# Kernel tuning notes

Measured on AMD Instinct MI355X. Metric: run time of the kernel, lower is better.

## Reference

```python
import jax, jax.numpy as jnp
import numpy as np

DIMS = 1024; HEAD = 16; HD = DIMS // HEAD
MAX_DIST = 1024; MAX_SPAN = 1024; TEMP_SCALE = 0.01
SCALE = HD ** -0.25  # hd^-0.25 per the torch modules


def _layer_norm(x, g, b, eps=1e-5):
    m = jnp.mean(x, -1, keepdims=True)
    v = jnp.mean((x - m) ** 2, -1, keepdims=True)
    return (x - m) * jax.lax.rsqrt(v + eps) * g + b


def _forward(x, ln_a_g, ln_a_b, ln_b_g, ln_b_b, Wq, bq, Wk, Wv, bv, Wc, bc, Wp, bp, Wo, bo):
    B, S, D = x.shape
    local = _layer_norm(x, ln_a_g, ln_a_b)
    globe = _layer_norm(x, ln_b_g, ln_b_b)
    # --- global path: QueryModule/KeyModule/ValueModule + AttentionCombiner SDPA (mask=None) ---
    q = (globe @ Wq.T + bq).reshape(B, S, HEAD, HD).transpose(0, 2, 1, 3) * SCALE
    k = (globe @ Wk.T).reshape(B, S, HEAD, HD).transpose(0, 2, 1, 3) * SCALE
    v = (globe @ Wv.T + bv).reshape(B, S, HEAD, HD).transpose(0, 2, 1, 3)
    # SDPA applies its own 1/sqrt(hd) on top of the modules' hd^-0.25 scalings (faithful to torch)
    scores = jnp.einsum('bhqd,bhkd->bhqk', q, k) / jnp.sqrt(jnp.asarray(HD, x.dtype))
    w = jax.nn.softmax(scores, -1)
    g_out = jnp.einsum('bhqk,bhkd->bhqd', w, v).transpose(0, 2, 1, 3).reshape(B, S, D)
    g_out = g_out @ Wc.T + bc
    # --- span predictor; torch uses span_scale.mean().item() which detaches -> stop_gradient ---
    span_scale = jax.nn.sigmoid(jnp.mean(g_out, 1) @ Wp.T + bp)  # [B,1]
    span_mean = jax.lax.stop_gradient(jnp.mean(span_scale))
    span_len = jnp.minimum(jnp.floor(MAX_SPAN * span_mean).astype(jnp.int32), S)
    eff = jnp.maximum(jnp.minimum(span_len, MAX_DIST), 1)  # eff_span (>=1 to keep softmax finite)
    temp = 1.0 + TEMP_SCALE * (1.0 - span_mean)  # sharpen=True branch
    # --- local AdaptiveSpan path: q[:, :eff], k[:, :eff], v[:, :eff] expressed as masking
    #     so shapes stay static under jit; rows >= eff are the zero-padding of the span output.
    lh = local.reshape(B, S, HEAD, HD).transpose(0, 2, 1, 3)  # [B,H,S,hd]
    ls = jnp.einsum('bhqd,bhkd->bhqk', lh, lh) / temp * SCALE
    valid = jnp.arange(S) < eff
    ls = jnp.where(valid[None, None, None, :], ls, jnp.asarray(-1e30, x.dtype))
    lw = jax.nn.softmax(ls, -1)
    l_out = jnp.einsum('bhqk,bhkd->bhqd', lw, lh).transpose(0, 2, 1, 3).reshape(B, S, D)
    l_out = jnp.where(valid[None, :, None], l_out, jnp.asarray(0.0, x.dtype))
    combined = jnp.concatenate([l_out, g_out], -1)  # [B,S,2D]
    return combined @ Wo.T + bo


def setup_inputs() -> dict:
    key = jax.random.key(0)
    ks = jax.random.split(key, 8)
    B, S = 2, 1024
    nrm = lambda k, sh, std=0.02: jax.random.normal(k, sh, jnp.float32) * std
    return {
        'x': jax.random.normal(ks[0], (B, S, DIMS), jnp.float32),
        'ln_a_g': jnp.ones(DIMS, jnp.float32), 'ln_a_b': jnp.zeros(DIMS, jnp.float32),
        'ln_b_g': jnp.ones(DIMS, jnp.float32), 'ln_b_b': jnp.zeros(DIMS, jnp.float32),
        'Wq': nrm(ks[1], (DIMS, DIMS)), 'bq': jnp.zeros(DIMS, jnp.float32),
        'Wk': nrm(ks[2], (DIMS, DIMS)),
        'Wv': nrm(ks[3], (DIMS, DIMS)), 'bv': jnp.zeros(DIMS, jnp.float32),
        'Wc': nrm(ks[4], (DIMS, DIMS)), 'bc': jnp.zeros(DIMS, jnp.float32),
        'Wp': nrm(ks[5], (1, DIMS), (2.0 / (DIMS + 1)) ** 0.5), 'bp': jnp.zeros(1, jnp.float32),
        'Wo': nrm(ks[6], (DIMS, 2 * DIMS)), 'bo': jnp.zeros(DIMS, jnp.float32),
    }


def reference(x, ln_a_g, ln_a_b, ln_b_g, ln_b_b, Wq, bq, Wk, Wv, bv, Wc, bc, Wp, bp, Wo, bo):
    return _forward(x, ln_a_g, ln_a_b, ln_b_g, ln_b_b, Wq, bq, Wk, Wv, bv, Wc, bc, Wp, bp, Wo, bo)
```

## Files before the change

### kernel.cpp

```cpp
#include <hip/hip_runtime.h>
#include <math.h>

#define S_LEN 1024
#define DIMS  1024
#define NHEAD 16
#define HD    64
#define BATCH 2
#define MROWS (BATCH * S_LEN)
#define LOG2E 1.44269504088896f

typedef unsigned short us;
typedef __attribute__((ext_vector_type(8))) __bf16 bf8_t;
typedef __attribute__((ext_vector_type(8))) unsigned short us8_t;
typedef __attribute__((ext_vector_type(4))) unsigned short us4_t;
typedef __attribute__((ext_vector_type(4))) float f32x4;
typedef __attribute__((ext_vector_type(4))) unsigned int u32x4;

static __device__ inline us f2bf(float f) {
    unsigned int u = __builtin_bit_cast(unsigned int, f);
    unsigned int r = u + 0x7fffu + ((u >> 16) & 1u);
    return (us)(r >> 16);
}
static __device__ inline float bf2f(us v) {
    unsigned int u = ((unsigned int)v) << 16;
    return __builtin_bit_cast(float, u);
}
static __device__ inline unsigned int pk2bf(float lo, float hi) {
    unsigned int r;
    asm("v_cvt_pk_bf16_f32 %0, %1, %2" : "=v"(r) : "v"(lo), "v"(hi));
    return r;
}
static __device__ inline f32x4 mfma16(us8_t a, us8_t b, f32x4 c) {
    return __builtin_amdgcn_mfma_f32_16x16x32_bf16(
        __builtin_bit_cast(bf8_t, a), __builtin_bit_cast(bf8_t, b), c, 0, 0, 0);
}
static __device__ __forceinline__ void gload16(const us* g, us* l) {
    __builtin_amdgcn_global_load_lds(
        (__attribute__((address_space(1))) void*)(g),
        (__attribute__((address_space(3))) void*)(l), 16, 0, 0);
}

__global__ __launch_bounds__(256) void prep_kernel(
    const float* __restrict__ s0, const float* __restrict__ s1,
    const float* __restrict__ s2, const float* __restrict__ s3,
    const float* __restrict__ s4,
    us* __restrict__ d0, us* __restrict__ d1, us* __restrict__ d2,
    us* __restrict__ d3, us* __restrict__ d4,
    const float* __restrict__ x,
    const float* __restrict__ ga, const float* __restrict__ ba,
    const float* __restrict__ gb, const float* __restrict__ bb,
    us* __restrict__ outA, us* __restrict__ outB,
    unsigned int* __restrict__ ctr)
{
    int bidx = blockIdx.x;
    int t = threadIdx.x;
    if (bidx == 0 && t == 0) *ctr = 0u;
    if (bidx < 6144) {
        const float* src; us* dst; int blk;
        if (bidx < 1024)      { src = s0; dst = d0; blk = bidx; }
        else if (bidx < 2048) { src = s1; dst = d1; blk = bidx - 1024; }
        else if (bidx < 3072) { src = s2; dst = d2; blk = bidx - 2048; }
        else if (bidx < 4096) { src = s3; dst = d3; blk = bidx - 3072; }
        else                  { src = s4; dst = d4; blk = bidx - 4096; }
        size_t idx = (size_t)blk * 1024 + t * 4;
        float4 v = *(const float4*)(src + idx);
        us4_t ot;
        ot[0] = f2bf(v.x); ot[1] = f2bf(v.y); ot[2] = f2bf(v.z); ot[3] = f2bf(v.w);
        *(us4_t*)(dst + idx) = ot;
        return;
    }
    int row = bidx - 6144;
    const float* xr = x + (size_t)row * DIMS;
    float4 v = *(const float4*)(xr + t * 4);
    float sum1 = v.x + v.y + v.z + v.w;
    float sumq = v.x * v.x + v.y * v.y + v.z * v.z + v.w * v.w;
#pragma unroll
    for (int o = 32; o > 0; o >>= 1) {
        sum1 += __shfl_down(sum1, o, 64);
        sumq += __shfl_down(sumq, o, 64);
    }
    __shared__ float rs[4], rq[4];
    int wid = t >> 6, lane = t & 63;
    if (lane == 0) { rs[wid] = sum1; rq[wid] = sumq; }
    __syncthreads();
    float T1 = rs[0] + rs[1] + rs[2] + rs[3];
    float T2 = rq[0] + rq[1] + rq[2] + rq[3];
    float mean = T1 * (1.0f / DIMS);
    float var  = T2 * (1.0f / DIMS) - mean * mean;
    float inv  = 1.0f / sqrtf(var + 1e-5f);
    float4 vga = *(const float4*)(ga + t * 4);
    float4 vba = *(const float4*)(ba + t * 4);
    float4 vgb = *(const float4*)(gb + t * 4);
    float4 vbb = *(const float4*)(bb + t * 4);
    float nx = (v.x - mean) * inv, ny = (v.y - mean) * inv;
    float nz = (v.z - mean) * inv, nw = (v.w - mean) * inv;
    us4_t oa, ob;
    oa[0] = f2bf(nx * vga.x + vba.x); oa[1] = f2bf(ny * vga.y + vba.y);
    oa[2] = f2bf(nz * vga.z + vba.z); oa[3] = f2bf(nw * vga.w + vba.w);
    ob[0] = f2bf(nx * vgb.x + vbb.x); ob[1] = f2bf(ny * vgb.y + vbb.y);
    ob[2] = f2bf(nz * vgb.z + vbb.z); ob[3] = f2bf(nw * vgb.w + vbb.w);
    *(us4_t*)(outA + (size_t)row * DIMS + t * 4) = oa;
    *(us4_t*)(outB + (size_t)row * DIMS + t * 4) = ob;
}

template <int OUTBF>
static __device__ __forceinline__ void gemm128g_body(
    const us* __restrict__ A, int lda,
    const us* __restrict__ W, int ldw,
    const float* __restrict__ bias,
    void* __restrict__ Cp, int ldc, int K,
    int bm, int bn, us* As, us* Bs)
{
    int tid = threadIdx.x;
    int w = tid >> 6, l = tid & 63, l15 = l & 15, lhi = l >> 4;
    int wr = w >> 1, wc = w & 1;
    f32x4 acc[4][2];
#pragma unroll
    for (int m = 0; m < 4; ++m) { acc[m][0] = (f32x4){0,0,0,0}; acc[m][1] = (f32x4){0,0,0,0}; }
    int lr8 = l >> 3, lc = l & 7;

    int nK = K >> 6;
    {
#pragma unroll
        for (int c = 0; c < 4; ++c) {
            int R0 = c * 32 + w * 8;
            int row = R0 + lr8;
            int col8 = lc ^ (row & 7);
            gload16(A + (size_t)(bm + row) * lda + col8 * 8, As + R0 * 64);
        }
#pragma unroll
        for (int c = 0; c < 2; ++c) {
            int R0 = c * 32 + w * 8;
            int row = R0 + lr8;
            int col8 = lc ^ (row & 7);
            gload16(W + (size_t)(bn + row) * ldw + col8 * 8, Bs + R0 * 64);
        }
    }
    for (int t = 0; t < nK; ++t) {
        int cur = t & 1;
        __syncthreads();
        if (t + 1 < nK) {
            int nxt = cur ^ 1;
            int kt = (t + 1) * 64;
#pragma unroll
            for (int c = 0; c < 4; ++c) {
                int R0 = c * 32 + w * 8;
                int row = R0 + lr8;
                int col8 = lc ^ (row & 7);
                gload16(A + (size_t)(bm + row) * lda + kt + col8 * 8,
                        As + nxt * (128 * 64) + R0 * 64);
            }
#pragma unroll
            for (int c = 0; c < 2; ++c) {
                int R0 = c * 32 + w * 8;
                int row = R0 + lr8;
                int col8 = lc ^ (row & 7);
                gload16(W + (size_t)(bn + row) * ldw + kt + col8 * 8,
                        Bs + nxt * (64 * 64) + R0 * 64);
            }
        }
        const us* Ab = As + cur * (128 * 64);
        const us* Bb = Bs + cur * (64 * 64);
#pragma unroll
        for (int kk = 0; kk < 2; ++kk) {
            int xo = ((kk * 4 + lhi) ^ (l15 & 7)) * 8;
            us8_t af[4], bfr[2];
#pragma unroll
            for (int m = 0; m < 4; ++m)
                af[m] = *(const us8_t*)&Ab[(wr * 64 + m * 16 + l15) * 64 + xo];
#pragma unroll
            for (int n = 0; n < 2; ++n)
                bfr[n] = *(const us8_t*)&Bb[(wc * 32 + n * 16 + l15) * 64 + xo];
#pragma unroll
            for (int m = 0; m < 4; ++m)
#pragma unroll
                for (int n = 0; n < 2; ++n)
                    acc[m][n] = mfma16(af[m], bfr[n], acc[m][n]);
        }
    }
    float bvv[2] = {0.f, 0.f};
    if (bias) {
#pragma unroll
        for (int n = 0; n < 2; ++n)
            bvv[n] = bias[bn + wc * 32 + n * 16 + l15];
    }
#pragma unroll
    for (int m = 0; m < 4; ++m) {
#pragma unroll
        for (int n = 0; n < 2; ++n) {
            int row = bm + wr * 64 + m * 16 + lhi * 4;
            int col = bn + wc * 32 + n * 16 + l15;
            if (OUTBF) {
                us* Cb = (us*)Cp;
                unsigned int p01 = pk2bf(acc[m][n][0] + bvv[n], acc[m][n][1] + bvv[n]);
                unsigned int p23 = pk2bf(acc[m][n][2] + bvv[n], acc[m][n][3] + bvv[n]);
                Cb[(size_t)(row + 0) * ldc + col] = (us)p01;
                Cb[(size_t)(row + 1) * ldc + col] = (us)(p01 >> 16);
                Cb[(size_t)(row + 2) * ldc + col] = (us)p23;
                Cb[(size_t)(row + 3) * ldc + col] = (us)(p23 >> 16);
            } else {
                float* Cf = (float*)Cp;
#pragma unroll
                for (int r = 0; r < 4; ++r)
                    Cf[(size_t)(row + r) * ldc + col] = acc[m][n][r] + bvv[n];
            }
        }
    }
}

__global__ __launch_bounds__(256) void gemm_qkv(
    const us* __restrict__ A,
    const us* __restrict__ Wq, const us* __restrict__ Wk, const us* __restrict__ Wv,
    const float* __restrict__ bq, const float* __restrict__ bv,
    us* __restrict__ qo, us* __restrict__ ko, us* __restrict__ vo)
{
    __shared__ __align__(16) us As[2][128 * 64];
    __shared__ __align__(16) us Bs[2][64 * 64];
    int which = blockIdx.x >> 4;
    int bn = (blockIdx.x & 15) * 64, bm = blockIdx.y * 128;
    const us* W = (which == 0) ? Wq : ((which == 1) ? Wk : Wv);
    const float* bias2 = (which == 0) ? bq : ((which == 2) ? bv : nullptr);
    us* Out = (which == 0) ? qo : ((which == 1) ? ko : vo);
    gemm128g_body<1>(A, DIMS, W, DIMS, bias2, Out, DIMS, DIMS, bm, bn,
                     &As[0][0], &Bs[0][0]);
}

template <int OUTBF>
__global__ __launch_bounds__(256) void gemm64g(
    const us* __restrict__ A, int lda,
    const us* __restrict__ W, int ldw,
    const float* __restrict__ bias,
    void* __restrict__ Cp, int ldc, int K)
{
    __shared__ __align__(16) us As[2][64 * 64];
    __shared__ __align__(16) us Bs[2][64 * 64];
    int tid = threadIdx.x;
    int w = tid >> 6, l = tid & 63, l15 = l & 15, lhi = l >> 4;
    int wr = w >> 1, wc = w & 1;
    int bm = blockIdx.y * 64, bn = blockIdx.x * 64;
    f32x4 acc[2][2] = {{{0,0,0,0},{0,0,0,0}},{{0,0,0,0},{0,0,0,0}}};
    int lr8 = l >> 3, lc = l & 7;

    int nK = K >> 6;
    {
#pragma unroll
        for (int c = 0; c < 2; ++c) {
            int R0 = c * 32 + w * 8;
            int row = R0 + lr8;
            int col8 = lc ^ (row & 7);
            gload16(A + (size_t)(bm + row) * lda + col8 * 8, &As[0][R0 * 64]);
            gload16(W + (size_t)(bn + row) * ldw + col8 * 8, &Bs[0][R0 * 64]);
        }
    }
    for (int t = 0; t < nK; ++t) {
        int cur = t & 1;
        __syncthreads();
        if (t + 1 < nK) {
            int nxt = cur ^ 1;
            int kt = (t + 1) * 64;
#pragma unroll
            for (int c = 0; c < 2; ++c) {
                int R0 = c * 32 + w * 8;
                int row = R0 + lr8;
                int col8 = lc ^ (row & 7);
                gload16(A + (size_t)(bm + row) * lda + kt + col8 * 8, &As[nxt][R0 * 64]);
                gload16(W + (size_t)(bn + row) * ldw + kt + col8 * 8, &Bs[nxt][R0 * 64]);
            }
        }
#pragma unroll
        for (int kk = 0; kk < 2; ++kk) {
            int xo = ((kk * 4 + lhi) ^ (l15 & 7)) * 8;
            us8_t af[2], bfr[2];
#pragma unroll
            for (int m = 0; m < 2; ++m)
                af[m] = *(const us8_t*)&As[cur][(wr * 32 + m * 16 + l15) * 64 + xo];
#pragma unroll
            for (int n = 0; n < 2; ++n)
                bfr[n] = *(const us8_t*)&Bs[cur][(wc * 32 + n * 16 + l15) * 64 + xo];
#pragma unroll
            for (int m = 0; m < 2; ++m)
#pragma unroll
                for (int n = 0; n < 2; ++n)
                    acc[m][n] = mfma16(af[m], bfr[n], acc[m][n]);
        }
    }
    float bvv[2] = {0.f, 0.f};
    if (bias) {
#pragma unroll
        for (int n = 0; n < 2; ++n)
            bvv[n] = bias[bn + wc * 32 + n * 16 + l15];
    }
#pragma unroll
    for (int m = 0; m < 2; ++m) {
#pragma unroll
        for (int n = 0; n < 2; ++n) {
            int row = bm + wr * 32 + m * 16 + lhi * 4;
            int col = bn + wc * 32 + n * 16 + l15;
            if (OUTBF) {
                us* Cb = (us*)Cp;
                unsigned int p01 = pk2bf(acc[m][n][0] + bvv[n], acc[m][n][1] + bvv[n]);
                unsigned int p23 = pk2bf(acc[m][n][2] + bvv[n], acc[m][n][3] + bvv[n]);
                Cb[(size_t)(row + 0) * ldc + col] = (us)p01;
                Cb[(size_t)(row + 1) * ldc + col] = (us)(p01 >> 16);
                Cb[(size_t)(row + 2) * ldc + col] = (us)p23;
                Cb[(size_t)(row + 3) * ldc + col] = (us)(p23 >> 16);
            } else {
                float* Cf = (float*)Cp;
#pragma unroll
                for (int r = 0; r < 4; ++r)
                    Cf[(size_t)(row + r) * ldc + col] = acc[m][n][r] + bvv[n];
            }
        }
    }
}

template <int LOCAL>
__global__ __launch_bounds__(512) void attn_mfma(
    const us* __restrict__ Q, const us* __restrict__ K,
    const us* __restrict__ V, us* __restrict__ O, int ldo,
    const float* __restrict__ span)
{
    __shared__ __align__(16) us Ks[2][64 * 64];
    __shared__ __align__(16) us Vt[2][64 * 64];
    __shared__ __align__(16) us Ps[8][1024];

    int bid = blockIdx.x;
    int xcd = bid & 7, slot = bid >> 3;
    int p = xcd + 8 * (slot >> 4);
    int q0blk = (slot & 15) * 64;
    int h = p & 15, b = p >> 4;

    int tid = threadIdx.x;
    int w = tid >> 6, l = tid & 63;
    int l15 = l & 15, lhi = l >> 4;
    int wq = w & 3, wk = w >> 2;

    float scale; int eff;
    if (LOCAL) { scale = span[1] * LOG2E; eff = (int)span[0]; }
    else       { scale = LOG2E / 64.0f; eff = S_LEN; }
    int ntiles = LOCAL ? ((eff + 63) >> 6) : 16;
    int nIter = (ntiles + 1) >> 1;

    int qrow = q0blk + wq * 16 + l15;
    const us* qptr = Q + ((size_t)(b * S_LEN + qrow)) * DIMS + h * HD + lhi * 8;
    us8_t qf[2];
    qf[0] = *(const us8_t*)(qptr);
    qf[1] = *(const us8_t*)(qptr + 32);

    f32x4 o[4] = {{0,0,0,0},{0,0,0,0},{0,0,0,0},{0,0,0,0}};
    float m_r[4] = {-1e30f, -1e30f, -1e30f, -1e30f};
    float l_r[4] = {0.f, 0.f, 0.f, 0.f};

    int half = tid >> 8;
    int t0 = tid & 255;
    int krow = t0 >> 3, kcol8 = t0 & 7;
    int ksl = (kcol8 ^ (krow & 7)) * 8;
    int vkb = t0 & 15, vdb = t0 >> 4;
    const us* Kb = K + ((size_t)(b * S_LEN)) * DIMS + h * HD;
    const us* Vb = V + ((size_t)(b * S_LEN)) * DIMS + h * HD;

    unsigned pbase = (unsigned)(unsigned long long)&Ps[w][0];
    unsigned paddr = pbase + (unsigned)(l * 8);

    us8_t kc0, kc1;
    us4_t vr0, vr1, vr2, vr3;
    if (half < ntiles) {
        const us* kp = Kb + (size_t)(half * 64 + krow) * DIMS + kcol8 * 8;
        kc0 = *(const us8_t*)kp;
        kc1 = *(const us8_t*)(kp + (size_t)32 * DIMS);
        const us* vp = Vb + (size_t)(half * 64 + vkb * 4) * DIMS + vdb * 4;
        vr0 = *(const us4_t*)(vp);
        vr1 = *(const us4_t*)(vp + DIMS);
        vr2 = *(const us4_t*)(vp + 2 * DIMS);
        vr3 = *(const us4_t*)(vp + 3 * DIMS);
    }

    for (int i = 0; i < nIter; ++i) {
        __syncthreads();
        if (2 * i + half < ntiles) {
            *(us8_t*)&Ks[half][krow * 64 + ksl] = kc0;
            *(us8_t*)&Ks[half][(krow + 32) * 64 + ksl] = kc1;
#pragma unroll
            for (int j = 0; j < 4; ++j) {
                int d = vdb * 4 + j;
                us4_t wv;
                wv[0] = vr0[j]; wv[1] = vr1[j]; wv[2] = vr2[j]; wv[3] = vr3[j];
                int slotv = (vkb >> 1) ^ (d & 7);
                *(us4_t*)&Vt[half][d * 64 + slotv * 8 + (vkb & 1) * 4] = wv;
            }
        }
        __syncthreads();
        int nt2 = 2 * (i + 1) + half;
        if (nt2 < ntiles) {
            const us* kp = Kb + (size_t)(nt2 * 64 + krow) * DIMS + kcol8 * 8;
            kc0 = *(const us8_t*)kp;
            kc1 = *(const us8_t*)(kp + (size_t)32 * DIMS);
            const us* vp = Vb + (size_t)(nt2 * 64 + vkb * 4) * DIMS + vdb * 4;
            vr0 = *(const us4_t*)(vp);
            vr1 = *(const us4_t*)(vp + DIMS);
            vr2 = *(const us4_t*)(vp + 2 * DIMS);
            vr3 = *(const us4_t*)(vp + 3 * DIMS);
        }
        int kt = 2 * i + wk;
        if (kt < ntiles) {
            f32x4 s4[4] = {{0,0,0,0},{0,0,0,0},{0,0,0,0},{0,0,0,0}};
            __builtin_amdgcn_s_setprio(1);
#pragma unroll
            for (int kk = 0; kk < 2; ++kk) {
                int xo = ((kk * 4 + lhi) ^ (l15 & 7)) * 8;
#pragma unroll
                for (int n = 0; n < 4; ++n) {
                    us8_t bk = *(const us8_t*)&Ks[wk][(n * 16 + l15) * 64 + xo];
                    s4[n] = mfma16(qf[kk], bk, s4[n]);
                }
            }
            __builtin_amdgcn_s_setprio(0);
#pragma unroll
            for (int n = 0; n < 4; ++n) {
                s4[n] *= scale;
                if (LOCAL) {
                    int key = kt * 64 + n * 16 + l15;
                    if (key >= eff) {
                        s4[n][0] = -1e30f; s4[n][1] = -1e30f;
                        s4[n][2] = -1e30f; s4[n][3] = -1e30f;
                    }
                }
            }
            float tl[4];
#pragma unroll
            for (int r = 0; r < 4; ++r)
                tl[r] = fmaxf(fmaxf(s4[0][r], s4[1][r]), fmaxf(s4[2][r], s4[3][r]));
            int ex = (tl[0] > m_r[0] + 11.5f) | (tl[1] > m_r[1] + 11.5f) |
                     (tl[2] > m_r[2] + 11.5f) | (tl[3] > m_r[3] + 11.5f);
            if (__any(ex)) {
#pragma unroll
                for (int msk = 1; msk <= 8; msk <<= 1) {
#pragma unroll
                    for (int r = 0; r < 4; ++r)
                        tl[r] = fmaxf(tl[r], __shfl_xor(tl[r], msk, 64));
                }
                float fac[4];
#pragma unroll
                for (int r = 0; r < 4; ++r) {
                    float mn = fmaxf(m_r[r], tl[r]);
                    fac[r] = exp2f(m_r[r] - mn);
                    m_r[r] = mn;
                    l_r[r] *= fac[r];
                }
#pragma unroll
                for (int n = 0; n < 4; ++n) {
                    o[n][0] *= fac[0]; o[n][1] *= fac[1];
                    o[n][2] *= fac[2]; o[n][3] *= fac[3];
                }
            }
#pragma unroll
            for (int n = 0; n < 4; ++n) {
                float p0 = exp2f(s4[n][0] - m_r[0]);
                float p1 = exp2f(s4[n][1] - m_r[1]);
                float p2 = exp2f(s4[n][2] - m_r[2]);
                float p3 = exp2f(s4[n][3] - m_r[3]);
                l_r[0] += p0; l_r[1] += p1; l_r[2] += p2; l_r[3] += p3;
                unsigned int p01 = pk2bf(p0, p1);
                unsigned int p23 = pk2bf(p2, p3);
                int idx = (n >> 1) * 512 + ((l15 & 4) ? 256 : 0)
                        + ((n & 1) * 2 + (l15 >> 3)) * 64 + (l15 & 3) * 16 + lhi * 4;
                *(uint2*)&Ps[w][idx] = make_uint2(p01, p23);
            }
            unsigned long long ta0, ta1, ta2, ta3;
            asm volatile(
                "ds_read_b64_tr_b16 %0, %4\n\t"
                "ds_read_b64_tr_b16 %1, %4 offset:512\n\t"
                "ds_read_b64_tr_b16 %2, %4 offset:1024\n\t"
                "ds_read_b64_tr_b16 %3, %4 offset:1536\n\t"
                "s_waitcnt lgkmcnt(0)"
                : "=&v"(ta0), "=&v"(ta1), "=&v"(ta2), "=&v"(ta3)
                : "v"(paddr)
                : "memory");
            __builtin_amdgcn_sched_barrier(0);
            u32x4 w0 = {(unsigned)ta0, (unsigned)(ta0 >> 32),
                        (unsigned)ta1, (unsigned)(ta1 >> 32)};
            u32x4 w1 = {(unsigned)ta2, (unsigned)(ta2 >> 32),
                        (unsigned)ta3, (unsigned)(ta3 >> 32)};
            us8_t pa0 = __builtin_bit_cast(us8_t, w0);
            us8_t pa1 = __builtin_bit_cast(us8_t, w1);
            __builtin_amdgcn_s_setprio(1);
#pragma unroll
            for (int kk = 0; kk < 2; ++kk) {
                int xo = ((kk * 4 + lhi) ^ (l15 & 7)) * 8;
                us8_t pa = kk ? pa1 : pa0;
#pragma unroll
                for (int n = 0; n < 4; ++n) {
                    us8_t vb = *(const us8_t*)&Vt[wk][(n * 16 + l15) * 64 + xo];
                    o[n] = mfma16(pa, vb, o[n]);
                }
            }
            __builtin_amdgcn_s_setprio(0);
        }
    }

#pragma unroll
    for (int msk = 1; msk <= 8; msk <<= 1) {
#pragma unroll
        for (int r = 0; r < 4; ++r)
            l_r[r] += __shfl_xor(l_r[r], msk, 64);
    }

    __syncthreads();
    float* obuf = (float*)&Ks[0][0];
    float* mlb  = (float*)&Vt[0][0];
    if (wk == 1) {
#pragma unroll
        for (int n = 0; n < 4; ++n)
#pragma unroll
            for (int r = 0; r < 4; ++r)
                obuf[wq * 1024 + (lhi * 4 + r) * 64 + n * 16 + l15] = o[n][r];
        if (l15 == 0) {
#pragma unroll
            for (int r = 0; r < 4; ++r) {
                mlb[wq * 32 + (lhi * 4 + r) * 2 + 0] = m_r[r];
                mlb[wq * 32 + (lhi * 4 + r) * 2 + 1] = l_r[r];
            }
        }
    }
    __syncthreads();
    if (wk == 0) {
        float f0[4], f1[4], rcp[4];
#pragma unroll
        for (int r = 0; r < 4; ++r) {
            int row = lhi * 4 + r;
            float m1 = mlb[wq * 32 + row * 2 + 0];
            float l1 = mlb[wq * 32 + row * 2 + 1];
            float ms = fmaxf(m_r[r], m1);
            f0[r] = exp2f(m_r[r] - ms);
            f1[r] = exp2f(m1 - ms);
            rcp[r] = 1.0f / (l_r[r] * f0[r] + l1 * f1[r]);
        }
#pragma unroll
        for (int n = 0; n < 4; ++n) {
            float vv[4];
#pragma unroll
            for (int r = 0; r < 4; ++r) {
                int row = q0blk + wq * 16 + lhi * 4 + r;
                float val = (o[n][r] * f0[r] +
                             obuf[wq * 1024 + (lhi * 4 + r) * 64 + n * 16 + l15] * f1[r]) * rcp[r];
                if (LOCAL && row >= eff) val = 0.0f;
                vv[r] = val;
            }
            int row0 = q0blk + wq * 16 + lhi * 4;
            unsigned int p01 = pk2bf(vv[0], vv[1]);
            unsigned int p23 = pk2bf(vv[2], vv[3]);
            size_t base = ((size_t)(b * S_LEN + row0)) * ldo + h * HD + n * 16 + l15;
            O[base + 0 * ldo] = (us)p01;
            O[base + 1 * ldo] = (us)(p01 >> 16);
            O[base + 2 * ldo] = (us)p23;
            O[base + 3 * ldo] = (us)(p23 >> 16);
        }
    }
}

__global__ __launch_bounds__(256) void span_fused(
    const us* __restrict__ gout, const float* __restrict__ Wp,
    const float* __restrict__ bp,
    float* __restrict__ partials, float* __restrict__ spanbuf,
    unsigned int* __restrict__ ctr)
{
    int slice = blockIdx.x;
    int b = blockIdx.y;
    int t = threadIdx.x;
    float4 wp = *(const float4*)(Wp + t * 4);
    float acc = 0;
    int srow0 = slice * 8;
    for (int s = srow0; s < srow0 + 8; ++s) {
        us4_t g = *(const us4_t*)(gout + (size_t)(b * S_LEN + s) * 2048 + t * 4);
        acc += bf2f(g[0]) * wp.x + bf2f(g[1]) * wp.y + bf2f(g[2]) * wp.z + bf2f(g[3]) * wp.w;
    }
#pragma unroll
    for (int o = 32; o > 0; o >>= 1) acc += __shfl_down(acc, o, 64);
    __shared__ float r[4];
    int wid = t >> 6, lane = t & 63;
    if (lane == 0) r[wid] = acc;
    __syncthreads();
    if (t == 0) {
        partials[b * 128 + slice] = r[0] + r[1] + r[2] + r[3];
        __threadfence();
        unsigned int old = atomicAdd(ctr, 1u);
        if (old == 255u) {
            __threadfence();
            float l0 = 0, l1 = 0;
            for (int i = 0; i < 128; ++i) { l0 += partials[i]; l1 += partials[128 + i]; }
            l0 = l0 * (1.0f / 1024.0f) + bp[0];
            l1 = l1 * (1.0f / 1024.0f) + bp[0];
            float sg0 = 1.0f / (1.0f + expf(-l0));
            float sg1 = 1.0f / (1.0f + expf(-l1));
            float sm = 0.5f * (sg0 + sg1);
            int sl = (int)floorf(1024.0f * sm);
            int eff = sl; if (eff > 1024) eff = 1024; if (eff < 1) eff = 1;
            float temp = 1.0f + 0.01f * (1.0f - sm);
            spanbuf[0] = (float)eff;
            spanbuf[1] = 0.35355339059327378f / temp;
        }
    }
}

extern "C" void kernel_launch(void* const* d_in, const int* in_sizes, int n_in,
                              void* d_out, int out_size, void* d_ws, size_t ws_size,
                              hipStream_t stream)
{
    (void)in_sizes; (void)n_in; (void)out_size; (void)ws_size;
    const float* x   = (const float*)d_in[0];
    const float* lag = (const float*)d_in[1];
    const float* lab = (const float*)d_in[2];
    const float* lbg = (const float*)d_in[3];
    const float* lbb = (const float*)d_in[4];
    const float* Wq  = (const float*)d_in[5];
    const float* bq  = (const float*)d_in[6];
    const float* Wk  = (const float*)d_in[7];
    const float* Wv  = (const float*)d_in[8];
    const float* bv  = (const float*)d_in[9];
    const float* Wc  = (const float*)d_in[10];
    const float* bc  = (const float*)d_in[11];
    const float* Wp  = (const float*)d_in[12];
    const float* bp  = (const float*)d_in[13];
    const float* Wo  = (const float*)d_in[14];
    const float* bo  = (const float*)d_in[15];
    float* out = (float*)d_out;
    us* wsu = (us*)d_ws;

    const size_t NM = (size_t)MROWS * DIMS;
    us* lnAbf = wsu;
    us* lnBbf = wsu + NM;
    us* gattbf = lnBbf;
    us* qbf   = wsu + 2 * NM;
    us* kbf   = wsu + 3 * NM;
    us* vbf   = wsu + 4 * NM;
    us* combbf = qbf;
    us* Wqbf  = wsu + 5 * NM;
    us* Wkbf  = Wqbf + DIMS * DIMS;
    us* Wvbf  = Wkbf + DIMS * DIMS;
    us* Wcbf  = Wvbf + DIMS * DIMS;
    us* Wobf  = Wcbf + DIMS * DIMS;
    float* partials = (float*)(Wobf + 2 * DIMS * DIMS);
    float* spanbuf  = partials + 256;
    unsigned int* spanctr = (unsigned int*)(spanbuf + 8);

    prep_kernel<<<8192, 256, 0, stream>>>(Wq, Wk, Wv, Wc, Wo,
                                          Wqbf, Wkbf, Wvbf, Wcbf, Wobf,
                                          x, lag, lab, lbg, lbb, lnAbf, lnBbf,
                                          spanctr);

    gemm_qkv<<<dim3(48, MROWS / 128), 256, 0, stream>>>(
        lnBbf, Wqbf, Wkbf, Wvbf, bq, bv, qbf, kbf, vbf);

    attn_mfma<0><<<512, 512, 0, stream>>>(qbf, kbf, vbf, gattbf, DIMS, nullptr);

    gemm64g<1><<<dim3(DIMS / 64, MROWS / 64), 256, 0, stream>>>(
        gattbf, DIMS, Wcbf, DIMS, bc, combbf + 1024, 2048, DIMS);

    span_fused<<<dim3(128, BATCH), 256, 0, stream>>>(combbf + 1024, Wp, bp,
                                                     partials, spanbuf, spanctr);

    attn_mfma<1><<<512, 512, 0, stream>>>(lnAbf, lnAbf, lnAbf, combbf, 2048, spanbuf);

    gemm64g<0><<<dim3(DIMS / 64, MROWS / 64), 256, 0, stream>>>(
        combbf, 2048, Wobf, 2048, bo, out, DIMS, 2 * DIMS);
}
```

Baseline: 128.3 us.

## Fuse span reduction into Wc GEMM and overlap local attention with Wo GEMM

Folds the span predictor's Wp dot product into the epilogue of the Wc projection GEMM, which removes the separate span kernel and its reread of the global output. The Wo projection is split by K half: the global half runs as extra blocks inside the local attention launch, and the local half runs afterwards and accumulates into the output. The aim is fewer launches and better GPU occupancy by running independent work concurrently. In exchange, the new Wo GEMM is single-buffered with no prefetch, and the read-modify-write accumulate adds extra fp32 traffic.

```diff
diff --git a/kernel.cpp b/kernel.cpp
--- a/kernel.cpp
+++ b/kernel.cpp
@@ -103,12 +103,11 @@
     *(us4_t*)(outB + (size_t)row * DIMS + t * 4) = ob;
 }
 
-template <int OUTBF>
 static __device__ __forceinline__ void gemm128g_body(
     const us* __restrict__ A, int lda,
     const us* __restrict__ W, int ldw,
     const float* __restrict__ bias,
-    void* __restrict__ Cp, int ldc, int K,
+    us* __restrict__ Cp, int ldc, int K,
     int bm, int bn, us* As, us* Bs)
 {
     int tid = threadIdx.x;
@@ -118,7 +117,6 @@
 #pragma unroll
     for (int m = 0; m < 4; ++m) { acc[m][0] = (f32x4){0,0,0,0}; acc[m][1] = (f32x4){0,0,0,0}; }
     int lr8 = l >> 3, lc = l & 7;
-
     int nK = K >> 6;
     {
 #pragma unroll
@@ -190,20 +188,12 @@
         for (int n = 0; n < 2; ++n) {
             int row = bm + wr * 64 + m * 16 + lhi * 4;
             int col = bn + wc * 32 + n * 16 + l15;
-            if (OUTBF) {
-                us* Cb = (us*)Cp;
-                unsigned int p01 = pk2bf(acc[m][n][0] + bvv[n], acc[m][n][1] + bvv[n]);
-                unsigned int p23 = pk2bf(acc[m][n][2] + bvv[n], acc[m][n][3] + bvv[n]);
-                Cb[(size_t)(row + 0) * ldc + col] = (us)p01;
-                Cb[(size_t)(row + 1) * ldc + col] = (us)(p01 >> 16);
-                Cb[(size_t)(row + 2) * ldc + col] = (us)p23;
-                Cb[(size_t)(row + 3) * ldc + col] = (us)(p23 >> 16);
-            } else {
-                float* Cf = (float*)Cp;
-#pragma unroll
-                for (int r = 0; r < 4; ++r)
-                    Cf[(size_t)(row + r) * ldc + col] = acc[m][n][r] + bvv[n];
-            }
+            unsigned int p01 = pk2bf(acc[m][n][0] + bvv[n], acc[m][n][1] + bvv[n]);
+            unsigned int p23 = pk2bf(acc[m][n][2] + bvv[n], acc[m][n][3] + bvv[n]);
+            Cp[(size_t)(row + 0) * ldc + col] = (us)p01;
+            Cp[(size_t)(row + 1) * ldc + col] = (us)(p01 >> 16);
+            Cp[(size_t)(row + 2) * ldc + col] = (us)p23;
+            Cp[(size_t)(row + 3) * ldc + col] = (us)(p23 >> 16);
         }
     }
 }
@@ -221,26 +211,27 @@
     const us* W = (which == 0) ? Wq : ((which == 1) ? Wk : Wv);
     const float* bias2 = (which == 0) ? bq : ((which == 2) ? bv : nullptr);
     us* Out = (which == 0) ? qo : ((which == 1) ? ko : vo);
-    gemm128g_body<1>(A, DIMS, W, DIMS, bias2, Out, DIMS, DIMS, bm, bn,
-                     &As[0][0], &Bs[0][0]);
-}
-
-template <int OUTBF>
-__global__ __launch_bounds__(256) void gemm64g(
-    const us* __restrict__ A, int lda,
-    const us* __restrict__ W, int ldw,
-    const float* __restrict__ bias,
-    void* __restrict__ Cp, int ldc, int K)
+    gemm128g_body(A, DIMS, W, DIMS, bias2, Out, DIMS, DIMS, bm, bn,
+                  &As[0][0], &Bs[0][0]);
+}
+
+__global__ __launch_bounds__(256) void gemm_wc_span(
+    const us* __restrict__ A, const us* __restrict__ W,
+    const float* __restrict__ bias, us* __restrict__ Cp,
+    const float* __restrict__ Wp, const float* __restrict__ bp,
+    float* __restrict__ partials, float* __restrict__ spanbuf,
+    unsigned int* __restrict__ ctr)
 {
     __shared__ __align__(16) us As[2][64 * 64];
     __shared__ __align__(16) us Bs[2][64 * 64];
+    __shared__ float red[4];
+    const int lda = DIMS, ldw = DIMS, ldc = 2048, K = DIMS;
     int tid = threadIdx.x;
     int w = tid >> 6, l = tid & 63, l15 = l & 15, lhi = l >> 4;
     int wr = w >> 1, wc = w & 1;
     int bm = blockIdx.y * 64, bn = blockIdx.x * 64;
     f32x4 acc[2][2] = {{{0,0,0,0},{0,0,0,0}},{{0,0,0,0},{0,0,0,0}}};
     int lr8 = l >> 3, lc = l & 7;
-
     int nK = K >> 6;
     {
 #pragma unroll
@@ -284,47 +275,71 @@
                     acc[m][n] = mfma16(af[m], bfr[n], acc[m][n]);
         }
     }
-    float bvv[2] = {0.f, 0.f};
-    if (bias) {
-#pragma unroll
-        for (int n = 0; n < 2; ++n)
-            bvv[n] = bias[bn + wc * 32 + n * 16 + l15];
-    }
+    float bvv[2], wpv[2];
+#pragma unroll
+    for (int n = 0; n < 2; ++n) {
+        int col = bn + wc * 32 + n * 16 + l15;
+        bvv[n] = bias[col];
+        wpv[n] = Wp[col];
+    }
+    float spart = 0.f;
 #pragma unroll
     for (int m = 0; m < 2; ++m) {
 #pragma unroll
         for (int n = 0; n < 2; ++n) {
             int row = bm + wr * 32 + m * 16 + lhi * 4;
             int col = bn + wc * 32 + n * 16 + l15;
-            if (OUTBF) {
-                us* Cb = (us*)Cp;
-                unsigned int p01 = pk2bf(acc[m][n][0] + bvv[n], acc[m][n][1] + bvv[n]);
-                unsigned int p23 = pk2bf(acc[m][n][2] + bvv[n], acc[m][n][3] + bvv[n]);
-                Cb[(size_t)(row + 0) * ldc + col] = (us)p01;
-                Cb[(size_t)(row + 1) * ldc + col] = (us)(p01 >> 16);
-                Cb[(size_t)(row + 2) * ldc + col] = (us)p23;
-                Cb[(size_t)(row + 3) * ldc + col] = (us)(p23 >> 16);
-            } else {
-                float* Cf = (float*)Cp;
-#pragma unroll
-                for (int r = 0; r < 4; ++r)
-                    Cf[(size_t)(row + r) * ldc + col] = acc[m][n][r] + bvv[n];
-            }
+            float v0 = acc[m][n][0] + bvv[n];
+            float v1 = acc[m][n][1] + bvv[n];
+            float v2 = acc[m][n][2] + bvv[n];
+            float v3 = acc[m][n][3] + bvv[n];
+            spart += (v0 + v1 + v2 + v3) * wpv[n];
+            unsigned int p01 = pk2bf(v0, v1);
+            unsigned int p23 = pk2bf(v2, v3);
+            Cp[(size_t)(row + 0) * ldc + col] = (us)p01;
+            Cp[(size_t)(row + 1) * ldc + col] = (us)(p01 >> 16);
+            Cp[(size_t)(row + 2) * ldc + col] = (us)p23;
+            Cp[(size_t)(row + 3) * ldc + col] = (us)(p23 >> 16);
+        }
+    }
+#pragma unroll
+    for (int msk = 1; msk <= 32; msk <<= 1)
+        spart += __shfl_xor(spart, msk, 64);
+    if (l == 0) red[w] = spart;
+    __syncthreads();
+    if (tid == 0) {
+        int blockid = blockIdx.y * 16 + blockIdx.x;
+        partials[blockid] = red[0] + red[1] + red[2] + red[3];
+        __threadfence();
+        unsigned int old = atomicAdd(ctr, 1u);
+        if (old == 511u) {
+            __threadfence();
+            float l0 = 0, l1 = 0;
+            for (int i = 0; i < 256; ++i) { l0 += partials[i]; l1 += partials[256 + i]; }
+            l0 = l0 * (1.0f / 1024.0f) + bp[0];
+            l1 = l1 * (1.0f / 1024.0f) + bp[0];
+            float sg0 = 1.0f / (1.0f + expf(-l0));
+            float sg1 = 1.0f / (1.0f + expf(-l1));
+            float sm = 0.5f * (sg0 + sg1);
+            int sl = (int)floorf(1024.0f * sm);
+            int eff = sl; if (eff > 1024) eff = 1024; if (eff < 1) eff = 1;
+            float temp = 1.0f + 0.01f * (1.0f - sm);
+            spanbuf[0] = (float)eff;
+            spanbuf[1] = 0.35355339059327378f / temp;
         }
     }
 }
 
 template <int LOCAL>
-__global__ __launch_bounds__(512) void attn_mfma(
+static __device__ __forceinline__ void attn_body(
     const us* __restrict__ Q, const us* __restrict__ K,
     const us* __restrict__ V, us* __restrict__ O, int ldo,
-    const float* __restrict__ span)
-{
-    __shared__ __align__(16) us Ks[2][64 * 64];
-    __shared__ __align__(16) us Vt[2][64 * 64];
-    __shared__ __align__(16) us Ps[8][1024];
-
-    int bid = blockIdx.x;
+    const float* __restrict__ span, us* smem, int bid)
+{
+    us* KsP = smem;
+    us* VtP = smem + 8192;
+    us* PsP = smem + 16384;
+
     int xcd = bid & 7, slot = bid >> 3;
     int p = xcd + 8 * (slot >> 4);
     int q0blk = (slot & 15) * 64;
@@ -359,7 +374,7 @@
     const us* Kb = K + ((size_t)(b * S_LEN)) * DIMS + h * HD;
     const us* Vb = V + ((size_t)(b * S_LEN)) * DIMS + h * HD;
 
-    unsigned pbase = (unsigned)(unsigned long long)&Ps[w][0];
+    unsigned pbase = (unsigned)(unsigned long long)&PsP[w * 1024];
     unsigned paddr = pbase + (unsigned)(l * 8);
 
     us8_t kc0, kc1;
@@ -378,15 +393,15 @@
     for (int i = 0; i < nIter; ++i) {
         __syncthreads();
         if (2 * i + half < ntiles) {
-            *(us8_t*)&Ks[half][krow * 64 + ksl] = kc0;
-            *(us8_t*)&Ks[half][(krow + 32) * 64 + ksl] = kc1;
+            *(us8_t*)&KsP[half * 4096 + krow * 64 + ksl] = kc0;
+            *(us8_t*)&KsP[half * 4096 + (krow + 32) * 64 + ksl] = kc1;
 #pragma unroll
             for (int j = 0; j < 4; ++j) {
                 int d = vdb * 4 + j;
                 us4_t wv;
                 wv[0] = vr0[j]; wv[1] = vr1[j]; wv[2] = vr2[j]; wv[3] = vr3[j];
                 int slotv = (vkb >> 1) ^ (d & 7);
-                *(us4_t*)&Vt[half][d * 64 + slotv * 8 + (vkb & 1) * 4] = wv;
+                *(us4_t*)&VtP[half * 4096 + d * 64 + slotv * 8 + (vkb & 1) * 4] = wv;
             }
         }
         __syncthreads();
@@ -410,7 +425,7 @@
                 int xo = ((kk * 4 + lhi) ^ (l15 & 7)) * 8;
 #pragma unroll
                 for (int n = 0; n < 4; ++n) {
-                    us8_t bk = *(const us8_t*)&Ks[wk][(n * 16 + l15) * 64 + xo];
+                    us8_t bk = *(const us8_t*)&KsP[wk * 4096 + (n * 16 + l15) * 64 + xo];
                     s4[n] = mfma16(qf[kk], bk, s4[n]);
                 }
             }
@@ -464,7 +479,7 @@
                 unsigned int p23 = pk2bf(p2, p3);
                 int idx = (n >> 1) * 512 + ((l15 & 4) ? 256 : 0)
                         + ((n & 1) * 2 + (l15 >> 3)) * 64 + (l15 & 3) * 16 + lhi * 4;
-                *(uint2*)&Ps[w][idx] = make_uint2(p01, p23);
+                *(uint2*)&PsP[w * 1024 + idx] = make_uint2(p01, p23);
             }
             unsigned long long ta0, ta1, ta2, ta3;
             asm volatile(
@@ -490,7 +505,7 @@
                 us8_t pa = kk ? pa1 : pa0;
 #pragma unroll
                 for (int n = 0; n < 4; ++n) {
-                    us8_t vb = *(const us8_t*)&Vt[wk][(n * 16 + l15) * 64 + xo];
+                    us8_t vb = *(const us8_t*)&VtP[wk * 4096 + (n * 16 + l15) * 64 + xo];
                     o[n] = mfma16(pa, vb, o[n]);
                 }
             }
@@ -506,8 +521,8 @@
     }
 
     __syncthreads();
-    float* obuf = (float*)&Ks[0][0];
-    float* mlb  = (float*)&Vt[0][0];
+    float* obuf = (float*)KsP;
+    float* mlb  = (float*)VtP;
     if (wk == 1) {
 #pragma unroll
         for (int n = 0; n < 4; ++n)
@@ -558,48 +573,105 @@
     }
 }
 
-__global__ __launch_bounds__(256) void span_fused(
-    const us* __restrict__ gout, const float* __restrict__ Wp,
-    const float* __restrict__ bp,
-    float* __restrict__ partials, float* __restrict__ spanbuf,
-    unsigned int* __restrict__ ctr)
-{
-    int slice = blockIdx.x;
-    int b = blockIdx.y;
-    int t = threadIdx.x;
-    float4 wp = *(const float4*)(Wp + t * 4);
-    float acc = 0;
-    int srow0 = slice * 8;
-    for (int s = srow0; s < srow0 + 8; ++s) {
-        us4_t g = *(const us4_t*)(gout + (size_t)(b * S_LEN + s) * 2048 + t * 4);
-        acc += bf2f(g[0]) * wp.x + bf2f(g[1]) * wp.y + bf2f(g[2]) * wp.z + bf2f(g[3]) * wp.w;
-    }
-#pragma unroll
-    for (int o = 32; o > 0; o >>= 1) acc += __shfl_down(acc, o, 64);
-    __shared__ float r[4];
-    int wid = t >> 6, lane = t & 63;
-    if (lane == 0) r[wid] = acc;
-    __syncthreads();
-    if (t == 0) {
-        partials[b * 128 + slice] = r[0] + r[1] + r[2] + r[3];
-        __threadfence();
-        unsigned int old = atomicAdd(ctr, 1u);
-        if (old == 255u) {
-            __threadfence();
-            float l0 = 0, l1 = 0;
-            for (int i = 0; i < 128; ++i) { l0 += partials[i]; l1 += partials[128 + i]; }
-            l0 = l0 * (1.0f / 1024.0f) + bp[0];
-            l1 = l1 * (1.0f / 1024.0f) + bp[0];
-            float sg0 = 1.0f / (1.0f + expf(-l0));
-            float sg1 = 1.0f / (1.0f + expf(-l1));
-            float sm = 0.5f * (sg0 + sg1);
-            int sl = (int)floorf(1024.0f * sm);
-            int eff = sl; if (eff > 1024) eff = 1024; if (eff < 1) eff = 1;
-            float temp = 1.0f + 0.01f * (1.0f - sm);
-            spanbuf[0] = (float)eff;
-            spanbuf[1] = 0.35355339059327378f / temp;
-        }
-    }
+__global__ __launch_bounds__(512) void attn_g_kernel(
+    const us* __restrict__ Q, const us* __restrict__ K,
+    const us* __restrict__ V, us* __restrict__ O)
+{
+    extern __shared__ us smem[];
+    attn_body<0>(Q, K, V, O, DIMS, nullptr, smem, blockIdx.x);
+}
+
+template <int ADDTO>
+static __device__ __forceinline__ void gemm_wo_body(
+    const us* __restrict__ A, const us* __restrict__ W,
+    const float* __restrict__ bias, float* __restrict__ C,
+    int K, int bm, int bn, us* As, us* Bs)
+{
+    int tid = threadIdx.x;
+    int w = tid >> 6, l = tid & 63, l15 = l & 15, lhi = l >> 4;
+    int wr = w >> 2, wc = w & 3;
+    f32x4 acc[4][2];
+#pragma unroll
+    for (int m = 0; m < 4; ++m) { acc[m][0] = (f32x4){0,0,0,0}; acc[m][1] = (f32x4){0,0,0,0}; }
+    int lr8 = l >> 3, lc = l & 7;
+    int nK = K >> 6;
+    for (int t = 0; t < nK; ++t) {
+        int kt = t * 64;
+        __syncthreads();
+#pragma unroll
+        for (int c = 0; c < 2; ++c) {
+            int R0 = c * 64 + w * 8;
+            int row = R0 + lr8;
+            int col8 = lc ^ (row & 7);
+            gload16(A + (size_t)(bm + row) * 2048 + kt + col8 * 8, As + R0 * 64);
+            gload16(W + (size_t)(bn + row) * 2048 + kt + col8 * 8, Bs + R0 * 64);
+        }
+        __syncthreads();
+#pragma unroll
+        for (int kk = 0; kk < 2; ++kk) {
+            int xo = ((kk * 4 + lhi) ^ (l15 & 7)) * 8;
+            us8_t af[4], bfr[2];
+#pragma unroll
+            for (int m = 0; m < 4; ++m)
+                af[m] = *(const us8_t*)&As[(wr * 64 + m * 16 + l15) * 64 + xo];
+#pragma unroll
+            for (int n = 0; n < 2; ++n)
+                bfr[n] = *(const us8_t*)&Bs[(wc * 32 + n * 16 + l15) * 64 + xo];
+#pragma unroll
+            for (int m = 0; m < 4; ++m)
+#pragma unroll
+                for (int n = 0; n < 2; ++n)
+                    acc[m][n] = mfma16(af[m], bfr[n], acc[m][n]);
+        }
+    }
+#pragma unroll
+    for (int m = 0; m < 4; ++m) {
+#pragma unroll
+        for (int n = 0; n < 2; ++n) {
+            int row = bm + wr * 64 + m * 16 + lhi * 4;
+            int col = bn + wc * 32 + n * 16 + l15;
+            if (ADDTO) {
+#pragma unroll
+                for (int r = 0; r < 4; ++r) {
+                    size_t idx = (size_t)(row + r) * 1024 + col;
+                    C[idx] = C[idx] + acc[m][n][r];
+                }
+            } else {
+                float bb = bias[col];
+#pragma unroll
+                for (int r = 0; r < 4; ++r)
+                    C[(size_t)(row + r) * 1024 + col] = acc[m][n][r] + bb;
+            }
+        }
+    }
+}
+
+__global__ __launch_bounds__(512) void attnl_wo(
+    const us* __restrict__ lnA, us* __restrict__ comb,
+    const float* __restrict__ span,
+    const us* __restrict__ Wo, const float* __restrict__ bo,
+    float* __restrict__ outp)
+{
+    extern __shared__ us smem[];
+    if (blockIdx.x < 512) {
+        attn_body<1>(lnA, lnA, lnA, comb, 2048, span, smem, blockIdx.x);
+    } else {
+        int gid = blockIdx.x - 512;
+        int bn = (gid & 7) * 128, bm = (gid >> 3) * 128;
+        gemm_wo_body<0>(comb + 1024, Wo + 1024, bo, outp, 1024, bm, bn,
+                        smem, smem + 128 * 64);
+    }
+}
+
+__global__ __launch_bounds__(512) void gemm_wo_left(
+    const us* __restrict__ comb, const us* __restrict__ Wo,
+    float* __restrict__ outp)
+{
+    extern __shared__ us smem[];
+    int gid = blockIdx.x;
+    int bn = (gid & 7) * 128, bm = (gid >> 3) * 128;
+    gemm_wo_body<1>(comb, Wo, nullptr, outp, 1024, bm, bn,
+                    smem, smem + 128 * 64);
 }
 
 extern "C" void kernel_launch(void* const* d_in, const int* in_sizes, int n_in,
@@ -640,7 +712,7 @@
     us* Wcbf  = Wvbf + DIMS * DIMS;
     us* Wobf  = Wcbf + DIMS * DIMS;
     float* partials = (float*)(Wobf + 2 * DIMS * DIMS);
-    float* spanbuf  = partials + 256;
+    float* spanbuf  = partials + 512;
     unsigned int* spanctr = (unsigned int*)(spanbuf + 8);
 
     prep_kernel<<<8192, 256, 0, stream>>>(Wq, Wk, Wv, Wc, Wo,
@@ -651,16 +723,12 @@
     gemm_qkv<<<dim3(48, MROWS / 128), 256, 0, stream>>>(
         lnBbf, Wqbf, Wkbf, Wvbf, bq, bv, qbf, kbf, vbf);
 
-    attn_mfma<0><<<512, 512, 0, stream>>>(qbf, kbf, vbf, gattbf, DIMS, nullptr);
-
-    gemm64g<1><<<dim3(DIMS / 64, MROWS / 64), 256, 0, stream>>>(
-        gattbf, DIMS, Wcbf, DIMS, bc, combbf + 1024, 2048, DIMS);
-
-    span_fused<<<dim3(128, BATCH), 256, 0, stream>>>(combbf + 1024, Wp, bp,
-                                                     partials, spanbuf, spanctr);
-
-    attn_mfma<1><<<512, 512, 0, stream>>>(lnAbf, lnAbf, lnAbf, combbf, 2048, spanbuf);
-
-    gemm64g<0><<<dim3(DIMS / 64, MROWS / 64), 256, 0, stream>>>(
-        combbf, 2048, Wobf, 2048, bo, out, DIMS, 2 * DIMS);
-}
+    attn_g_kernel<<<512, 512, 49152, stream>>>(qbf, kbf, vbf, gattbf);
+
+    gemm_wc_span<<<dim3(16, 32), 256, 0, stream>>>(
+        gattbf, Wcbf, bc, combbf + 1024, Wp, bp, partials, spanbuf, spanctr);
+
+    attnl_wo<<<640, 512, 49152, stream>>>(lnAbf, combbf, spanbuf, Wobf, bo, out);
+
+    gemm_wo_left<<<128, 512, 32768, stream>>>(combbf, Wobf, out);
+}
```

After: 144.2 us. 12.4% more time.
